# Performance work log

Measured on AMD Instinct MI355X. Metric: run time of the kernel, lower is better.

The kernel has to match this reference:

```python
import jax, jax.numpy as jnp
import numpy as np

N = 50000          # nodes (num_sensors)
E = 600000         # edges
IN_DIM = 75        # 3 * 25
DIMS = [(75, 128), (128, 128), (128, 32)]  # (in, out) per layer: in->hidden->hidden->bottleneck


def setup_inputs() -> dict:
    key = jax.random.key(0)
    ks = jax.random.split(key, 4 + 5 * len(DIMS))
    inp = {
        "x": jax.random.normal(ks[0], (N, IN_DIM), dtype=jnp.float32),
        "edge_index": jax.random.randint(ks[1], (2, E), 0, N, dtype=jnp.int64),
        "weight": jax.random.uniform(ks[2], (E,), dtype=jnp.float32),
        "sim": jax.random.normal(ks[3], (E, 2), dtype=jnp.float32),
    }
    i = 4
    for l, (cin, cout) in enumerate(DIMS):
        s = jnp.float32(1.0 / np.sqrt(cin))
        inp[f"wr{l}"] = jax.random.normal(ks[i + 0], (cin, cout), dtype=jnp.float32) * s  # real part of complex conv filter
        inp[f"wi{l}"] = jax.random.normal(ks[i + 1], (cin, cout), dtype=jnp.float32) * s  # imag part
        inp[f"cb{l}"] = jnp.zeros((cout,), dtype=jnp.float32)                              # conv bias
        inp[f"lw{l}"] = jax.random.normal(ks[i + 2], (cout, cin), dtype=jnp.float32) * s  # Linear weight (torch layout [out,in])
        inp[f"lb{l}"] = jnp.zeros((cout,), dtype=jnp.float32)                              # Linear bias
        i += 5
    return inp


def _layer(x, src, dst, cr, ci, wr, wi, cb, lw, lb):
    # ModeConvFast: gather source features, scale by complex edge coefficient
    # c = weight * (sim_r + i*sim_i), scatter-add to destination nodes,
    # project with complex filter W = wr + i*wi, keep real part, add bias.
    xs = x[src]                                   # [E, Cin] gather
    agg_r = jax.ops.segment_sum(xs * cr[:, None], dst, num_segments=N)  # [N, Cin]
    agg_i = jax.ops.segment_sum(xs * ci[:, None], dst, num_segments=N)  # [N, Cin]
    conv = agg_r @ wr - agg_i @ wi + cb           # real part of complex matmul
    return jax.nn.relu(conv + x @ lw.T + lb)      # conv(x,...) + lin(x), then relu


def reference(x, edge_index, weight, sim,
              wr0, wi0, cb0, lw0, lb0,
              wr1, wi1, cb1, lw1, lb1,
              wr2, wi2, cb2, lw2, lb2):
    src, dst = edge_index[0], edge_index[1]
    cr = weight * sim[:, 0]                       # [E] real edge coefficient
    ci = weight * sim[:, 1]                       # [E] imag edge coefficient
    layers = [
        (wr0, wi0, cb0, lw0, lb0),
        (wr1, wi1, cb1, lw1, lb1),
        (wr2, wi2, cb2, lw2, lb2),
    ]
    for p in layers:
        x = _layer(x, src, dst, cr, ci, *p)
    return x
```

## Files before the change

### kernel.cpp

```cpp
#include <hip/hip_runtime.h>

#define N_NODES 50000
#define N_EDGES 600000
#define E_PAD_MAX (N_EDGES + N_NODES * 7)

using bf16x8 = __attribute__((ext_vector_type(8))) short;
using f32x4  = __attribute__((ext_vector_type(4))) float;
typedef unsigned int uint32_tt;

__device__ __forceinline__ unsigned short f2bf(float f) {
    union { float f; unsigned int u; } v; v.f = f;
    unsigned int u = v.u;
    return (unsigned short)((u + 0x7fffu + ((u >> 16) & 1u)) >> 16);
}
__device__ __forceinline__ float bf2f(unsigned int h16) {
    union { unsigned int u; float f; } v; v.u = h16 << 16;
    return v.f;
}

__global__ void prep_kernel(
    const float* __restrict__ x0, unsigned short* __restrict__ xb,
    const float* __restrict__ wr0, const float* __restrict__ wi0,
    const float* __restrict__ lw0, unsigned short* __restrict__ BT0,
    const float* __restrict__ wr1, const float* __restrict__ wi1,
    const float* __restrict__ lw1, unsigned short* __restrict__ BT1,
    const float* __restrict__ wr2, const float* __restrict__ wi2,
    const float* __restrict__ lw2, unsigned short* __restrict__ BT2,
    int* __restrict__ cnt, uint2* __restrict__ edat, int n) {
    int tid = blockIdx.x * 256 + threadIdx.x;
    int nth = gridDim.x * 256;
    for (int i = tid; i < N_NODES; i += nth) cnt[i] = 0;
    uint2 z; z.x = 0u; z.y = 0u;
    for (int i = tid; i < E_PAD_MAX; i += nth) edat[i] = z;

    int i = tid;
    int nconv = n * 96;
    if (i < nconv) {
        int r = i / 96, c = i - r * 96;
        xb[i] = (c < 75) ? f2bf(x0[r * 75 + c]) : (unsigned short)0;
        return;
    }
    i -= nconv;
    if (i < 128 * 288) {
        int nn = i / 288, k = i - nn * 288;
        int part = k / 96, kk = k - part * 96;
        float v = 0.f;
        if (kk < 75) {
            if (part == 0)      v = wr0[kk * 128 + nn];
            else if (part == 1) v = -wi0[kk * 128 + nn];
            else                v = lw0[nn * 75 + kk];
        }
        BT0[i] = f2bf(v);
        return;
    }
    i -= 128 * 288;
    if (i < 128 * 384) {
        int nn = i / 384, k = i - nn * 384;
        int part = k >> 7, kk = k & 127;
        float v;
        if (part == 0)      v = wr1[kk * 128 + nn];
        else if (part == 1) v = -wi1[kk * 128 + nn];
        else                v = lw1[nn * 128 + kk];
        BT1[i] = f2bf(v);
        return;
    }
    i -= 128 * 384;
    if (i < 96 * 128) {
        int nn = i >> 7, k = i & 127;
        float v;
        if (nn < 32)      v = wr2[k * 32 + nn];
        else if (nn < 64) v = -wi2[k * 32 + (nn - 32)];
        else              v = lw2[(nn - 64) * 128 + k];
        BT2[i] = f2bf(v);
    }
}


__global__ void hist_kernel(const int* __restrict__ ei, int* __restrict__ cnt,
                            int* __restrict__ rank, int E) {
    int e = blockIdx.x * 256 + threadIdx.x;
    if (e < E) rank[e] = atomicAdd(&cnt[ei[E + e]], 1);
}

__global__ void scan1(const int* __restrict__ deg, int* __restrict__ out,
                      int* __restrict__ bsum, int n) {
    __shared__ int s[256];
    int t = threadIdx.x;
    int base = blockIdx.x * 1024 + t * 4;
    int v0 = (base + 0 < n) ? ((deg[base + 0] + 7) & ~7) : 0;
    int v1 = (base + 1 < n) ? ((deg[base + 1] + 7) & ~7) : 0;
    int v2 = (base + 2 < n) ? ((deg[base + 2] + 7) & ~7) : 0;
    int v3 = (base + 3 < n) ? ((deg[base + 3] + 7) & ~7) : 0;
    int tsum = v0 + v1 + v2 + v3;
    s[t] = tsum;
    __syncthreads();
    for (int off = 1; off < 256; off <<= 1) {
        int tmp = (t >= off) ? s[t - off] : 0;
        __syncthreads();
        s[t] += tmp;
        __syncthreads();
    }
    int excl = s[t] - tsum;
    if (base + 0 < n) out[base + 0] = excl;
    if (base + 1 < n) out[base + 1] = excl + v0;
    if (base + 2 < n) out[base + 2] = excl + v0 + v1;
    if (base + 3 < n) out[base + 3] = excl + v0 + v1 + v2;
    if (t == 255) bsum[blockIdx.x] = s[255];
}

__global__ void scan3(int* __restrict__ off, const int* __restrict__ bsum,
                      int n, int nb) {
    __shared__ int sp;
    int b = blockIdx.x, t = threadIdx.x;
    int seg = b >> 2;
    if (t == 0) {
        int acc = 0;
        for (int k = 0; k < seg; ++k) acc += bsum[k];
        sp = acc;
    }
    __syncthreads();
    int i = b * 256 + t;
    if (i < n) off[i] += sp;
    if (i == n) {
        int tot = sp;
        for (int k = seg; k < nb; ++k) tot += bsum[k];
        off[n] = tot;
    }
}

__global__ void scatter_kernel(const int* __restrict__ ei, const float* __restrict__ w,
                               const float* __restrict__ sim, const int* __restrict__ off,
                               const int* __restrict__ rank, uint2* __restrict__ edat,
                               int E) {
    int e = blockIdx.x * 256 + threadIdx.x;
    if (e >= E) return;
    int s = ei[e], d = ei[E + e];
    int p = off[d] + rank[e];
    float wt = w[e];
    uint2 m;
    m.x = (unsigned)s;
    m.y = (uint32_tt)f2bf(wt * sim[2 * e]) |
          ((uint32_tt)f2bf(wt * sim[2 * e + 1]) << 16);
    edat[p] = m;
}

template <int CU2>
__global__ __launch_bounds__(256) void agg_bf16(
    const uint32_tt* __restrict__ x, const int* __restrict__ off,
    const uint2* __restrict__ edat, uint32_tt* __restrict__ aggR,
    uint32_tt* __restrict__ aggI, int n) {
    int wave = threadIdx.x >> 6;
    int lane = threadIdx.x & 63;
    int node = __builtin_amdgcn_readfirstlane(blockIdx.x * 4 + wave);
    if (node >= n) return;
    int lc = (CU2 == 64) ? lane : (lane < CU2 ? lane : CU2 - 1);
    float arl = 0.f, arh = 0.f, ail = 0.f, aih = 0.f;
    int e0 = __builtin_amdgcn_readfirstlane(off[node]);
    int e1 = __builtin_amdgcn_readfirstlane(off[node + 1]);

    if (e0 < e1) {
        uint2 mn[8];
        int sc[8]; float crc[8], cic[8];
        uint32_tt wc[8];
        {
            uint2 m0[8];
#pragma unroll
            for (int j = 0; j < 8; ++j) m0[j] = edat[e0 + j];
#pragma unroll
            for (int j = 0; j < 8; ++j) {
                sc[j] = __builtin_amdgcn_readfirstlane((int)m0[j].x);
                int pk = __builtin_amdgcn_readfirstlane((int)m0[j].y);
                crc[j] = bf2f((unsigned)pk & 0xffffu);
                cic[j] = bf2f((unsigned)pk >> 16);
            }
            int nb = (e0 + 8 < e1) ? e0 + 8 : e0;
#pragma unroll
            for (int j = 0; j < 8; ++j) mn[j] = edat[nb + j];
#pragma unroll
            for (int j = 0; j < 8; ++j) wc[j] = x[(size_t)sc[j] * CU2 + lc];
        }
        for (int e = e0;; e += 8) {
            bool more = (e + 8 < e1);
            int sn[8]; float crn[8], cin_[8]; uint32_tt wn[8];
            if (more) {
#pragma unroll
                for (int j = 0; j < 8; ++j) {
                    sn[j] = __builtin_amdgcn_readfirstlane((int)mn[j].x);
                    int pk = __builtin_amdgcn_readfirstlane((int)mn[j].y);
                    crn[j] = bf2f((unsigned)pk & 0xffffu);
                    cin_[j] = bf2f((unsigned)pk >> 16);
                }
                int nb = (e + 16 < e1) ? e + 16 : e + 8;
#pragma unroll
                for (int j = 0; j < 8; ++j) mn[j] = edat[nb + j];
#pragma unroll
                for (int j = 0; j < 8; ++j) wn[j] = x[(size_t)sn[j] * CU2 + lc];
            }
#pragma unroll
            for (int j = 0; j < 8; ++j) {
                float lo = bf2f(wc[j] & 0xffffu), hi = bf2f(wc[j] >> 16);
                arl += crc[j] * lo; arh += crc[j] * hi;
                ail += cic[j] * lo; aih += cic[j] * hi;
            }
            if (!more) break;
#pragma unroll
            for (int j = 0; j < 8; ++j) {
                sc[j] = sn[j]; crc[j] = crn[j]; cic[j] = cin_[j]; wc[j] = wn[j];
            }
        }
    }
    if (lane < CU2) {
        aggR[(size_t)node * CU2 + lane] = (uint32_tt)f2bf(arl) | ((uint32_tt)f2bf(arh) << 16);
        aggI[(size_t)node * CU2 + lane] = (uint32_tt)f2bf(ail) | ((uint32_tt)f2bf(aih) << 16);
    }
}

__global__ __launch_bounds__(256) void agg_out(
    const uint32_tt* __restrict__ Y, const int* __restrict__ off,
    const uint2* __restrict__ edat, const float* __restrict__ cb,
    const float* __restrict__ lb, float* __restrict__ out, int n) {
    int wave = threadIdx.x >> 6;
    int lane = threadIdx.x & 63;
    int node = __builtin_amdgcn_readfirstlane(blockIdx.x * 4 + wave);
    if (node >= n) return;
    int lc = (lane < 32) ? lane : 31;
    int usei = (lane >> 4) & 1;
    float alo = 0.f, ahi = 0.f;
    int e0 = __builtin_amdgcn_readfirstlane(off[node]);
    int e1 = __builtin_amdgcn_readfirstlane(off[node + 1]);

    if (e0 < e1) {
        uint2 mn[8];
        int sc[8]; float crc[8], cic[8];
        uint32_tt wc[8];
        {
            uint2 m0[8];
#pragma unroll
            for (int j = 0; j < 8; ++j) m0[j] = edat[e0 + j];
#pragma unroll
            for (int j = 0; j < 8; ++j) {
                sc[j] = __builtin_amdgcn_readfirstlane((int)m0[j].x);
                int pk = __builtin_amdgcn_readfirstlane((int)m0[j].y);
                crc[j] = bf2f((unsigned)pk & 0xffffu);
                cic[j] = bf2f((unsigned)pk >> 16);
            }
            int nb = (e0 + 8 < e1) ? e0 + 8 : e0;
#pragma unroll
            for (int j = 0; j < 8; ++j) mn[j] = edat[nb + j];
#pragma unroll
            for (int j = 0; j < 8; ++j) wc[j] = Y[(size_t)sc[j] * 48 + lc];
        }
        for (int e = e0;; e += 8) {
            bool more = (e + 8 < e1);
            int sn[8]; float crn[8], cin_[8]; uint32_tt wn[8];
            if (more) {
#pragma unroll
                for (int j = 0; j < 8; ++j) {
                    sn[j] = __builtin_amdgcn_readfirstlane((int)mn[j].x);
                    int pk = __builtin_amdgcn_readfirstlane((int)mn[j].y);
                    crn[j] = bf2f((unsigned)pk & 0xffffu);
                    cin_[j] = bf2f((unsigned)pk >> 16);
                }
                int nb = (e + 16 < e1) ? e + 16 : e + 8;
#pragma unroll
                for (int j = 0; j < 8; ++j) mn[j] = edat[nb + j];
#pragma unroll
                for (int j = 0; j < 8; ++j) wn[j] = Y[(size_t)sn[j] * 48 + lc];
            }
#pragma unroll
            for (int j = 0; j < 8; ++j) {
                float c = usei ? cic[j] : crc[j];
                float lo = bf2f(wc[j] & 0xffffu), hi = bf2f(wc[j] >> 16);
                alo += c * lo; ahi += c * hi;
            }
            if (!more) break;
#pragma unroll
            for (int j = 0; j < 8; ++j) {
                sc[j] = sn[j]; crc[j] = crn[j]; cic[j] = cin_[j]; wc[j] = wn[j];
            }
        }
    }
    alo += __shfl_xor(alo, 16);
    ahi += __shfl_xor(ahi, 16);
    if (lane < 16) {
        uint32_tt lin = Y[(size_t)node * 48 + 32 + lane];
        int c0 = 2 * lane, c1 = 2 * lane + 1;
        float v0 = alo + bf2f(lin & 0xffffu) + cb[c0] + lb[c0];
        float v1 = ahi + bf2f(lin >> 16) + cb[c1] + lb[c1];
        float2 r;
        r.x = v0 > 0.f ? v0 : 0.f;
        r.y = v1 > 0.f ? v1 : 0.f;
        ((float2*)out)[(size_t)node * 16 + lane] = r;
    }
}

template <int CINP, int COUT, int BM, int WM, int WN, int MT, int NT,
          bool OUT_BF16, bool RAW, int PARTS>
__global__ __launch_bounds__(256) void gemm_mfma(
    const unsigned short* __restrict__ A0, const unsigned short* __restrict__ A1,
    const unsigned short* __restrict__ A2, const unsigned short* __restrict__ BT,
    const float* __restrict__ cb, const float* __restrict__ lb,
    void* __restrict__ outv, int n) {
    constexpr int PK = 40;
    constexpr int KTOT = PARTS * CINP;
    constexpr int NCH = KTOT / 32;
    constexpr int CPP = CINP / 32;
    __shared__ unsigned short sA[BM][PK];
    __shared__ unsigned short sB[COUT][PK];

    int t = threadIdx.x;
    int lane = t & 63, wave = t >> 6;
    int wm = wave / WN, wn = wave % WN;
    int ml = lane & 15, kh = lane >> 4;
    int node0 = blockIdx.x * BM;

    const unsigned short* Asrc[3] = {A0, A1, A2};

    f32x4 acc[MT][NT];
#pragma unroll
    for (int mt = 0; mt < MT; ++mt)
#pragma unroll
        for (int nt = 0; nt < NT; ++nt) acc[mt][nt] = (f32x4){0.f, 0.f, 0.f, 0.f};

    for (int c = 0; c < NCH; ++c) {
        int part = (PARTS == 1) ? 0 : (c / CPP);
        int kk = (c - part * CPP) * 32;
        const unsigned short* __restrict__ Ap = Asrc[part];
        __syncthreads();
#pragma unroll
        for (int i = t; i < BM * 4; i += 256) {
            int r = i >> 2, q = i & 3;
            int node = node0 + r;
            if (node >= n) node = n - 1;
            *(uint4*)&sA[r][q * 8] =
                *(const uint4*)(Ap + (size_t)node * CINP + kk + q * 8);
        }
#pragma unroll
        for (int i = t; i < COUT * 4; i += 256) {
            int r = i >> 2, q = i & 3;
            *(uint4*)&sB[r][q * 8] =
                *(const uint4*)(BT + (size_t)r * KTOT + c * 32 + q * 8);
        }
        __syncthreads();
        bf16x8 af[MT], bfr[NT];
#pragma unroll
        for (int mt = 0; mt < MT; ++mt)
            af[mt] = *(const bf16x8*)&sA[wm * (MT * 16) + mt * 16 + ml][kh * 8];
#pragma unroll
        for (int nt = 0; nt < NT; ++nt)
            bfr[nt] = *(const bf16x8*)&sB[wn * (NT * 16) + nt * 16 + ml][kh * 8];
#pragma unroll
        for (int mt = 0; mt < MT; ++mt)
#pragma unroll
            for (int nt = 0; nt < NT; ++nt)
                acc[mt][nt] = __builtin_amdgcn_mfma_f32_16x16x32_bf16(
                    af[mt], bfr[nt], acc[mt][nt], 0, 0, 0);
    }

    int row0 = kh * 4;
#pragma unroll
    for (int nt = 0; nt < NT; ++nt) {
        int col = wn * (NT * 16) + nt * 16 + ml;
        float bias = RAW ? 0.f : (cb[col] + lb[col]);
#pragma unroll
        for (int mt = 0; mt < MT; ++mt) {
#pragma unroll
            for (int r = 0; r < 4; ++r) {
                int node = node0 + wm * (MT * 16) + mt * 16 + row0 + r;
                if (node < n) {
                    float v = acc[mt][nt][r] + bias;
                    if (!RAW) v = v > 0.f ? v : 0.f;
                    if (OUT_BF16)
                        ((unsigned short*)outv)[(size_t)node * COUT + col] = f2bf(v);
                    else
                        ((float*)outv)[(size_t)node * COUT + col] = v;
                }
            }
        }
    }
}

__global__ __launch_bounds__(256) void gemm_l1y(
    const unsigned short* __restrict__ A0, const unsigned short* __restrict__ A1,
    const unsigned short* __restrict__ A2, const unsigned short* __restrict__ BT,
    const unsigned short* __restrict__ BT2, const float* __restrict__ cb,
    const float* __restrict__ lb, unsigned short* __restrict__ Yout, int n) {
    constexpr int PK = 40;
    constexpr int PH = 136;
    __shared__ unsigned short sA[128][PK];
    __shared__ unsigned short sB[128][PK];
    __shared__ unsigned short sH[128][PH];

    int t = threadIdx.x;
    int lane = t & 63, wave = t >> 6;
    int wm = wave >> 1, wn = wave & 1;
    int ml = lane & 15, kh = lane >> 4;
    int node0 = blockIdx.x * 128;
    const unsigned short* Asrc[3] = {A0, A1, A2};

    f32x4 acc[4][4];
#pragma unroll
    for (int mt = 0; mt < 4; ++mt)
#pragma unroll
        for (int nt = 0; nt < 4; ++nt) acc[mt][nt] = (f32x4){0.f, 0.f, 0.f, 0.f};

    for (int c = 0; c < 12; ++c) {
        int part = c >> 2;
        int kk = (c & 3) * 32;
        const unsigned short* __restrict__ Ap = Asrc[part];
        __syncthreads();
#pragma unroll
        for (int i = t; i < 512; i += 256) {
            int r = i >> 2, q = i & 3;
            int node = node0 + r;
            if (node >= n) node = n - 1;
            *(uint4*)&sA[r][q * 8] =
                *(const uint4*)(Ap + (size_t)node * 128 + kk + q * 8);
        }
#pragma unroll
        for (int i = t; i < 512; i += 256) {
            int r = i >> 2, q = i & 3;
            *(uint4*)&sB[r][q * 8] =
                *(const uint4*)(BT + (size_t)r * 384 + c * 32 + q * 8);
        }
        __syncthreads();
        bf16x8 af[4], bfr[4];
#pragma unroll
        for (int mt = 0; mt < 4; ++mt)
            af[mt] = *(const bf16x8*)&sA[wm * 64 + mt * 16 + ml][kh * 8];
#pragma unroll
        for (int nt = 0; nt < 4; ++nt)
            bfr[nt] = *(const bf16x8*)&sB[wn * 64 + nt * 16 + ml][kh * 8];
#pragma unroll
        for (int mt = 0; mt < 4; ++mt)
#pragma unroll
            for (int nt = 0; nt < 4; ++nt)
                acc[mt][nt] = __builtin_amdgcn_mfma_f32_16x16x32_bf16(
                    af[mt], bfr[nt], acc[mt][nt], 0, 0, 0);
    }

    int row0 = kh * 4;
#pragma unroll
    for (int nt = 0; nt < 4; ++nt) {
        int col = wn * 64 + nt * 16 + ml;
        float bias = cb[col] + lb[col];
#pragma unroll
        for (int mt = 0; mt < 4; ++mt) {
#pragma unroll
            for (int r = 0; r < 4; ++r) {
                int nl = wm * 64 + mt * 16 + row0 + r;
                float v = acc[mt][nt][r] + bias;
                sH[nl][col] = f2bf(v > 0.f ? v : 0.f);
            }
        }
    }
    __syncthreads();

    f32x4 acc2[4][3];
#pragma unroll
    for (int mt = 0; mt < 4; ++mt)
#pragma unroll
        for (int nt = 0; nt < 3; ++nt) acc2[mt][nt] = (f32x4){0.f, 0.f, 0.f, 0.f};
    for (int c2 = 0; c2 < 4; ++c2) {
        bf16x8 af[4], bfr[3];
#pragma unroll
        for (int mt = 0; mt < 4; ++mt)
            af[mt] = *(const bf16x8*)&sH[wm * 64 + mt * 16 + ml][c2 * 32 + kh * 8];
#pragma unroll
        for (int nt = 0; nt < 3; ++nt) {
            int ycol = wn * 48 + nt * 16 + ml;
            bfr[nt] = *(const bf16x8*)(BT2 + (size_t)ycol * 128 + c2 * 32 + kh * 8);
        }
#pragma unroll
        for (int mt = 0; mt < 4; ++mt)
#pragma unroll
            for (int nt = 0; nt < 3; ++nt)
                acc2[mt][nt] = __builtin_amdgcn_mfma_f32_16x16x32_bf16(
                    af[mt], bfr[nt], acc2[mt][nt], 0, 0, 0);
    }
#pragma unroll
    for (int nt = 0; nt < 3; ++nt) {
        int ycol = wn * 48 + nt * 16 + ml;
#pragma unroll
        for (int mt = 0; mt < 4; ++mt) {
#pragma unroll
            for (int r = 0; r < 4; ++r) {
                int node = node0 + wm * 64 + mt * 16 + row0 + r;
                if (node < n)
                    Yout[(size_t)node * 96 + ycol] = f2bf(acc2[mt][nt][r]);
            }
        }
    }
}


extern "C" void kernel_launch(void* const* d_in, const int* in_sizes, int n_in,
                              void* d_out, int out_size, void* d_ws, size_t ws_size,
                              hipStream_t stream) {
    const float* x0  = (const float*)d_in[0];
    const int*   ei  = (const int*)d_in[1];
    const float* wgt = (const float*)d_in[2];
    const float* sim = (const float*)d_in[3];
    const float *wr[3], *wi[3], *cb[3], *lw[3], *lb[3];
    for (int l = 0; l < 3; ++l) {
        wr[l] = (const float*)d_in[4 + 5 * l];
        wi[l] = (const float*)d_in[5 + 5 * l];
        cb[l] = (const float*)d_in[6 + 5 * l];
        lw[l] = (const float*)d_in[7 + 5 * l];
        lb[l] = (const float*)d_in[8 + 5 * l];
    }

    char* p = (char*)d_ws;
    auto alloc = [&](size_t bytes) -> void* {
        void* r = p;
        p += (bytes + 255) & ~(size_t)255;
        return r;
    };
    int*   off  = (int*)alloc((N_NODES + 1) * 4);
    int*   cnt  = (int*)alloc(N_NODES * 4);
    int*   bsum = (int*)alloc(256);
    int*   rank = (int*)alloc((size_t)N_EDGES * 4);
    uint2* edat = (uint2*)alloc((size_t)E_PAD_MAX * 8);
    unsigned short* xb    = (unsigned short*)alloc((size_t)N_NODES * 96 * 2);
    unsigned short* aggRb = (unsigned short*)alloc((size_t)N_NODES * 128 * 2);
    unsigned short* aggIb = (unsigned short*)alloc((size_t)N_NODES * 128 * 2);
    unsigned short* h1b   = (unsigned short*)alloc((size_t)N_NODES * 128 * 2);
    unsigned short* Yb    = (unsigned short*)alloc((size_t)N_NODES * 96 * 2);
    unsigned short* BT0   = (unsigned short*)alloc((size_t)128 * 288 * 2);
    unsigned short* BT1   = (unsigned short*)alloc((size_t)128 * 384 * 2);
    unsigned short* BT2   = (unsigned short*)alloc((size_t)96 * 128 * 2);
    float* outp = (float*)d_out;

    {
        int total = N_NODES * 96 + 128 * 288 + 128 * 384 + 96 * 128;
        prep_kernel<<<(total + 255) / 256, 256, 0, stream>>>(
            x0, xb, wr[0], wi[0], lw[0], BT0, wr[1], wi[1], lw[1], BT1,
            wr[2], wi[2], lw[2], BT2, cnt, edat, N_NODES);
    }
    hist_kernel<<<(N_EDGES + 255) / 256, 256, 0, stream>>>(ei, cnt, rank, N_EDGES);
    int nb = (N_NODES + 1023) / 1024;
    scan1<<<nb, 256, 0, stream>>>(cnt, off, bsum, N_NODES);
    scan3<<<(N_NODES + 1 + 255) / 256, 256, 0, stream>>>(off, bsum, N_NODES, nb);
    scatter_kernel<<<(N_EDGES + 255) / 256, 256, 0, stream>>>(ei, wgt, sim, off, rank,
                                                              edat, N_EDGES);

    int agrid = (N_NODES + 3) / 4;

    agg_bf16<48><<<agrid, 256, 0, stream>>>((const uint32_tt*)xb, off, edat,
                                            (uint32_tt*)aggRb, (uint32_tt*)aggIb, N_NODES);
    gemm_mfma<96, 128, 128, 2, 2, 4, 4, true, false, 3>
        <<<(N_NODES + 127) / 128, 256, 0, stream>>>(aggRb, aggIb, xb, BT0, cb[0], lb[0],
                                                    h1b, N_NODES);
    agg_bf16<64><<<agrid, 256, 0, stream>>>((const uint32_tt*)h1b, off, edat,
                                            (uint32_tt*)aggRb, (uint32_tt*)aggIb, N_NODES);
    gemm_l1y<<<(N_NODES + 127) / 128, 256, 0, stream>>>(aggRb, aggIb, h1b, BT1, BT2,
                                                        cb[1], lb[1], Yb, N_NODES);
    agg_out<<<agrid, 256, 0, stream>>>((const uint32_tt*)Yb, off, edat, cb[2], lb[2],
                                       outp, N_NODES);
}
```

Baseline: 260.3 us.

## Split each node's edge aggregation across two waves and reduce via LDS

The aggregation kernels now assign two wavefronts per destination node, each handling half of the 8-edge batches, and combine the partial sums through shared memory after a block barrier. This doubles the wave-level parallelism and shortens each wave's serial dependency chain of gathers. In exchange it adds a __syncthreads, LDS traffic, twice as many blocks, and idle waves for nodes with few edges. The bounds check on node was removed, which relies on N being even.

```diff
diff --git a/kernel.cpp b/kernel.cpp
--- a/kernel.cpp
+++ b/kernel.cpp
@@ -149,14 +149,19 @@
     const uint32_tt* __restrict__ x, const int* __restrict__ off,
     const uint2* __restrict__ edat, uint32_tt* __restrict__ aggR,
     uint32_tt* __restrict__ aggI, int n) {
+    __shared__ float part[2][4][64];
     int wave = threadIdx.x >> 6;
     int lane = threadIdx.x & 63;
-    int node = __builtin_amdgcn_readfirstlane(blockIdx.x * 4 + wave);
-    if (node >= n) return;
+    int pair = wave >> 1, half = wave & 1;
+    int node = __builtin_amdgcn_readfirstlane(blockIdx.x * 2 + pair);
     int lc = (CU2 == 64) ? lane : (lane < CU2 ? lane : CU2 - 1);
     float arl = 0.f, arh = 0.f, ail = 0.f, aih = 0.f;
-    int e0 = __builtin_amdgcn_readfirstlane(off[node]);
-    int e1 = __builtin_amdgcn_readfirstlane(off[node + 1]);
+    int eb = __builtin_amdgcn_readfirstlane(off[node]);
+    int ee = __builtin_amdgcn_readfirstlane(off[node + 1]);
+    int nbat = (ee - eb) >> 3;
+    int b0 = (nbat + 1) >> 1;
+    int e0 = half ? eb + b0 * 8 : eb;
+    int e1 = half ? ee : eb + b0 * 8;
 
     if (e0 < e1) {
         uint2 mn[8];
@@ -209,7 +214,14 @@
             }
         }
     }
-    if (lane < CU2) {
+    if (half) {
+        part[pair][0][lane] = arl; part[pair][1][lane] = arh;
+        part[pair][2][lane] = ail; part[pair][3][lane] = aih;
+    }
+    __syncthreads();
+    if (!half && lane < CU2) {
+        arl += part[pair][0][lane]; arh += part[pair][1][lane];
+        ail += part[pair][2][lane]; aih += part[pair][3][lane];
         aggR[(size_t)node * CU2 + lane] = (uint32_tt)f2bf(arl) | ((uint32_tt)f2bf(arh) << 16);
         aggI[(size_t)node * CU2 + lane] = (uint32_tt)f2bf(ail) | ((uint32_tt)f2bf(aih) << 16);
     }
@@ -219,15 +231,20 @@
     const uint32_tt* __restrict__ Y, const int* __restrict__ off,
     const uint2* __restrict__ edat, const float* __restrict__ cb,
     const float* __restrict__ lb, float* __restrict__ out, int n) {
+    __shared__ float part[2][2][64];
     int wave = threadIdx.x >> 6;
     int lane = threadIdx.x & 63;
-    int node = __builtin_amdgcn_readfirstlane(blockIdx.x * 4 + wave);
-    if (node >= n) return;
+    int pair = wave >> 1, half = wave & 1;
+    int node = __builtin_amdgcn_readfirstlane(blockIdx.x * 2 + pair);
     int lc = (lane < 32) ? lane : 31;
     int usei = (lane >> 4) & 1;
     float alo = 0.f, ahi = 0.f;
-    int e0 = __builtin_amdgcn_readfirstlane(off[node]);
-    int e1 = __builtin_amdgcn_readfirstlane(off[node + 1]);
+    int eb = __builtin_amdgcn_readfirstlane(off[node]);
+    int ee = __builtin_amdgcn_readfirstlane(off[node + 1]);
+    int nbat = (ee - eb) >> 3;
+    int b0 = (nbat + 1) >> 1;
+    int e0 = half ? eb + b0 * 8 : eb;
+    int e1 = half ? ee : eb + b0 * 8;
 
     if (e0 < e1) {
         uint2 mn[8];
@@ -280,17 +297,26 @@
             }
         }
     }
-    alo += __shfl_xor(alo, 16);
-    ahi += __shfl_xor(ahi, 16);
-    if (lane < 16) {
-        uint32_tt lin = Y[(size_t)node * 48 + 32 + lane];
-        int c0 = 2 * lane, c1 = 2 * lane + 1;
-        float v0 = alo + bf2f(lin & 0xffffu) + cb[c0] + lb[c0];
-        float v1 = ahi + bf2f(lin >> 16) + cb[c1] + lb[c1];
-        float2 r;
-        r.x = v0 > 0.f ? v0 : 0.f;
-        r.y = v1 > 0.f ? v1 : 0.f;
-        ((float2*)out)[(size_t)node * 16 + lane] = r;
+    if (half) {
+        part[pair][0][lane] = alo;
+        part[pair][1][lane] = ahi;
+    }
+    __syncthreads();
+    if (!half) {
+        alo += part[pair][0][lane];
+        ahi += part[pair][1][lane];
+        alo += __shfl_xor(alo, 16);
+        ahi += __shfl_xor(ahi, 16);
+        if (lane < 16) {
+            uint32_tt lin = Y[(size_t)node * 48 + 32 + lane];
+            int c0 = 2 * lane, c1 = 2 * lane + 1;
+            float v0 = alo + bf2f(lin & 0xffffu) + cb[c0] + lb[c0];
+            float v1 = ahi + bf2f(lin >> 16) + cb[c1] + lb[c1];
+            float2 r;
+            r.x = v0 > 0.f ? v0 : 0.f;
+            r.y = v1 > 0.f ? v1 : 0.f;
+            ((float2*)out)[(size_t)node * 16 + lane] = r;
+        }
     }
 }
 
@@ -544,7 +570,7 @@
     scatter_kernel<<<(N_EDGES + 255) / 256, 256, 0, stream>>>(ei, wgt, sim, off, rank,
                                                               edat, N_EDGES);
 
-    int agrid = (N_NODES + 3) / 4;
+    int agrid = N_NODES / 2;
 
     agg_bf16<48><<<agrid, 256, 0, stream>>>((const uint32_tt*)xb, off, edat,
                                             (uint32_tt*)aggRb, (uint32_tt*)aggIb, N_NODES);
```

After: 304.6 us. 17.0% more time.
